# Performance work log

Measured on AMD Instinct MI355X. Metric: run time of the kernel, lower is better.

The kernel has to match this reference:

```python
import jax, jax.numpy as jnp
import numpy as np

D_MODEL = 384
D_STATE = 64
D_CONV = 3
EXPAND = 2
HEADDIM = 64
NGROUPS = 1
CHUNK = 256
D_INNER = EXPAND * D_MODEL            # 768
NHEADS = D_INNER // HEADDIM           # 12
CONV_DIM = D_INNER + 2 * NGROUPS * D_STATE   # 896
D_IN_PROJ = 2 * D_INNER + 2 * NGROUPS * D_STATE + NHEADS  # 1676
EPS = 1e-5


def setup_inputs() -> dict:
    key = jax.random.key(0)
    ks = jax.random.split(key, 8)
    B, H, W = 16, 32, 32
    u = jax.random.normal(ks[0], (B, D_MODEL, H, W), jnp.float32)
    in_proj_w = jax.random.normal(ks[1], (D_IN_PROJ, D_MODEL), jnp.float32) / np.sqrt(D_MODEL)
    conv_w = jax.random.normal(ks[2], (CONV_DIM, 1, D_CONV, D_CONV), jnp.float32) / np.sqrt(D_CONV * D_CONV)
    conv_b = jax.random.normal(ks[3], (CONV_DIM,), jnp.float32) * 0.01
    # dt_bias init as in Mamba2.__init__
    dt = jnp.exp(jax.random.uniform(ks[4], (NHEADS,)) * (np.log(0.1) - np.log(0.001)) + np.log(0.001))
    dt = jnp.clip(dt, 1e-4, None)
    dt_bias = dt + jnp.log(-jnp.expm1(-dt))
    A_log = jnp.log(jax.random.uniform(ks[5], (NHEADS,), minval=1.0, maxval=16.0))
    D = jnp.ones((NHEADS,), jnp.float32)
    norm_w = jnp.ones((D_INNER,), jnp.float32)
    norm_b = jnp.zeros((D_INNER,), jnp.float32)
    out_proj_w = jax.random.normal(ks[6], (D_MODEL, D_INNER), jnp.float32) / np.sqrt(D_INNER)
    return {"u": u, "in_proj_w": in_proj_w, "conv_w": conv_w, "conv_b": conv_b,
            "dt_bias": dt_bias, "A_log": A_log, "D": D, "norm_w": norm_w,
            "norm_b": norm_b, "out_proj_w": out_proj_w}


def _chunk_scan(x, dt, A, Bm, Cm):
    """SSD chunked scan. x:(b,l,h,p) dt:(b,l,h) A:(h,) Bm,Cm:(b,l,g,n) -> (b,l,h,p)"""
    b, l, h, p = x.shape
    nc = l // CHUNK
    xc = x.reshape(b, nc, CHUNK, h, p)
    dtc = dt.reshape(b, nc, CHUNK, h)
    hpg = h // NGROUPS
    Bh = jnp.repeat(Bm.reshape(b, nc, CHUNK, NGROUPS, D_STATE), hpg, axis=3)  # (b,c,cs,h,n)
    Ch = jnp.repeat(Cm.reshape(b, nc, CHUNK, NGROUPS, D_STATE), hpg, axis=3)
    dA = dtc * A                                  # (b,c,cs,h)
    dA_cs = jnp.cumsum(dA, axis=2)                # cumulative log-decay within chunk
    # ---- intra-chunk (masked, attention-like) ----
    Lmat = jnp.exp(dA_cs[:, :, :, None, :] - dA_cs[:, :, None, :, :])  # (b,c,i,j,h)
    causal = jnp.tril(jnp.ones((CHUNK, CHUNK), bool))
    att = jnp.einsum('bcihn,bcjhn->bcijh', Ch, Bh) * Lmat * dtc[:, :, None, :, :]
    att = jnp.where(causal[None, None, :, :, None], att, 0.0)
    y_intra = jnp.einsum('bcijh,bcjhp->bcihp', att, xc)
    # ---- per-chunk end states ----
    decay_to_end = jnp.exp(dA_cs[:, :, -1:, :] - dA_cs)                 # (b,c,cs,h)
    states = jnp.einsum('bcjhn,bcjh,bcjhp->bchpn', Bh, decay_to_end * dtc, xc)
    chunk_decay = jnp.exp(dA_cs[:, :, -1, :])                           # (b,c,h)
    # ---- inter-chunk recurrence over the (few) chunks ----
    def step(carry, inp):
        st, dec = inp
        new = carry * dec[:, :, None, None] + st
        return new, carry  # emit state *before* this chunk
    init = jnp.zeros((b, h, p, D_STATE), x.dtype)
    _, prevs = jax.lax.scan(step, init, (jnp.moveaxis(states, 1, 0), jnp.moveaxis(chunk_decay, 1, 0)))
    prev_states = jnp.moveaxis(prevs, 0, 1)                             # (b,c,h,p,n)
    y_inter = jnp.einsum('bcihn,bcih,bchpn->bcihp', Ch, jnp.exp(dA_cs), prev_states)
    return (y_intra + y_inter).reshape(b, l, h, p)


def reference(u, in_proj_w, conv_w, conv_b, dt_bias, A_log, D, norm_w, norm_b, out_proj_w):
    B, C, H, W = u.shape
    L = H * W
    useq = u.reshape(B, C, L).transpose(0, 2, 1)                        # (B,L,C)
    zxbcdt = useq @ in_proj_w.T                                         # (B,L,D_IN_PROJ)
    z = zxbcdt[..., :D_INNER]
    xBC = zxbcdt[..., D_INNER:D_INNER + CONV_DIM]
    dt = jax.nn.softplus(zxbcdt[..., D_INNER + CONV_DIM:] + dt_bias)    # (B,L,NHEADS)
    # depthwise 3x3 conv over (H,W)
    xBC = xBC.reshape(B, H, W, CONV_DIM)
    kern = jnp.transpose(conv_w, (2, 3, 1, 0))                          # HWIO, groups=CONV_DIM
    xBC = jax.lax.conv_general_dilated(xBC, kern, (1, 1), 'SAME',
                                       dimension_numbers=('NHWC', 'HWIO', 'NHWC'),
                                       feature_group_count=CONV_DIM) + conv_b
    xBC = jax.nn.silu(xBC).reshape(B, L, CONV_DIM)
    x = xBC[..., :D_INNER].reshape(B, L, NHEADS, HEADDIM)
    Bm = xBC[..., D_INNER:D_INNER + NGROUPS * D_STATE].reshape(B, L, NGROUPS, D_STATE)
    Cm = xBC[..., D_INNER + NGROUPS * D_STATE:].reshape(B, L, NGROUPS, D_STATE)
    A = -jnp.exp(A_log)
    y = _chunk_scan(x, dt, A, Bm, Cm) + D[None, None, :, None] * x      # D skip per head
    y = y.reshape(B, L, D_INNER)
    # LayerNorm then gate by z (no activation on z, matching source)
    mu = jnp.mean(y, axis=-1, keepdims=True)
    var = jnp.var(y, axis=-1, keepdims=True)
    y = (y - mu) / jnp.sqrt(var + EPS) * norm_w + norm_b
    y = y * z
    out = y @ out_proj_w.T                                              # (B,L,C)
    return out.reshape(B, H, W, C).transpose(0, 3, 1, 2)
```

## Files before the change

kernel.cpp:

```cpp
#include <hip/hip_runtime.h>
#include <hip/hip_bf16.h>

#define B_    16
#define L_    1024
#define DM    384
#define DIP   1676
#define NIP   1664
#define DI    768
#define CONVD 896
#define NH    12
#define HD    64
#define DS    64
#define NCH   4
#define CH    256
#define EPS_  1e-5f

typedef unsigned short u16;
typedef unsigned int   u32;
typedef __attribute__((ext_vector_type(8))) _Float16 f16x8;
typedef __attribute__((ext_vector_type(4))) float f32x4;

union U4 { uint4 v; u16 s[8]; };

#define SWZ(row, slot) (((row) << 7) + ((((slot) ^ ((row) & 7)) & 7) << 4))

__device__ __forceinline__ u16 f2h(float v) { return __builtin_bit_cast(u16, (_Float16)v); }
__device__ __forceinline__ float h2f(u16 h) { return (float)__builtin_bit_cast(_Float16, h); }
__device__ __forceinline__ void hsplit(float v, u16& h, u16& l) {
  _Float16 hh = (_Float16)v;
  _Float16 ll = (_Float16)(v - (float)hh);
  h = __builtin_bit_cast(u16, hh);
  l = __builtin_bit_cast(u16, ll);
}

__global__ __launch_bounds__(256) void k_cvtA(const float* __restrict__ u,
                                              u16* __restrict__ Ah)
{
  __shared__ float Ls[32][129];
  const int t  = threadIdx.x;
  const int l0 = blockIdx.x * 128;
  const int k0 = blockIdx.y * 32;
  const int b  = blockIdx.z;
#pragma unroll
  for (int r = 0; r < 4; ++r) {
    int idx = r * 256 + t;
    int kk = idx >> 5, q = idx & 31;
    float4 v = *(const float4*)&u[((size_t)(b * DM + k0 + kk)) * L_ + l0 + q * 4];
    Ls[kk][q * 4 + 0] = v.x; Ls[kk][q * 4 + 1] = v.y;
    Ls[kk][q * 4 + 2] = v.z; Ls[kk][q * 4 + 3] = v.w;
  }
  __syncthreads();
#pragma unroll
  for (int it = 0; it < 2; ++it) {
    int task = it * 256 + t;
    int l = task >> 2, kq = (task & 3) * 8;
    u32 hw[4];
#pragma unroll
    for (int j = 0; j < 4; ++j) {
      u16 h0 = f2h(Ls[kq + 2 * j + 0][l]);
      u16 h1 = f2h(Ls[kq + 2 * j + 1][l]);
      hw[j] = (u32)h0 | ((u32)h1 << 16);
    }
    size_t off = ((size_t)(b * L_ + l0 + l)) * DM + k0 + kq;
    *(uint4*)&Ah[off] = make_uint4(hw[0], hw[1], hw[2], hw[3]);
  }
}

__global__ __launch_bounds__(256) void k_cvtWh(const float* __restrict__ W,
                                               u16* __restrict__ Wh, int total4)
{
  int i = blockIdx.x * 256 + threadIdx.x;
  if (i >= total4) return;
  int e = i * 4;
  float4 v = *(const float4*)&W[e];
  u16 h[4] = {f2h(v.x), f2h(v.y), f2h(v.z), f2h(v.w)};
  *(uint2*)&Wh[e] = make_uint2((u32)h[0] | ((u32)h[1] << 16), (u32)h[2] | ((u32)h[3] << 16));
}

__global__ __launch_bounds__(256) void k_dtp(
    const float* __restrict__ u, const float* __restrict__ ipw,
    const float* __restrict__ dtb, const float* __restrict__ A_log,
    float* __restrict__ dt, float* __restrict__ dAcs, float* __restrict__ cdecay)
{
  __shared__ float wdt[DM];
  __shared__ float ws4[4];
  const int bc = blockIdx.x;
  const int h  = blockIdx.y;
  const int b  = bc >> 2, l0 = (bc & 3) * 256;
  const int t  = threadIdx.x;
  const int lane = t & 63, w = t >> 6;
  for (int i = t; i < DM; i += 256) wdt[i] = ipw[(size_t)(NIP + h) * DM + i];
  __syncthreads();
  const float* ub = u + (size_t)b * DM * L_ + l0 + t;
  float acc = 0.f;
#pragma unroll 8
  for (int k = 0; k < DM; ++k)
    acc = fmaf(ub[(size_t)k * L_], wdt[k], acc);
  const size_t row = (size_t)bc * 256 + t;
  float logit = acc + dtb[h];
  float dtv = (logit > 20.f) ? logit : log1pf(expf(logit));
  dt[row * NH + h] = dtv;
  float xv = dtv * (-expf(A_log[h]));
#pragma unroll
  for (int off = 1; off < 64; off <<= 1) {
    float y = __shfl_up(xv, off, 64);
    if (lane >= off) xv += y;
  }
  if (lane == 63) ws4[w] = xv;
  __syncthreads();
  float add = 0.f;
#pragma unroll
  for (int i = 0; i < 4; ++i) if (i < w) add += ws4[i];
  xv += add;
  dAcs[row * NH + h] = xv;
  if (t == 255) cdecay[bc * NH + h] = expf(xv);
}

#define STAGE2(bufbase, k0) do {                                                                \
  _Pragma("unroll")                                                                             \
  for (int i_ = 0; i_ < 2; ++i_) {                                                              \
    int S_ = i_ * 256 + t;                                                                      \
    int m_ = S_ >> 2;                                                                           \
    int g_ = (S_ ^ (m_ >> 1)) & 3;                                                              \
    size_t goff_ = (size_t)m_ * DM + (k0) + g_ * 8;                                             \
    __builtin_amdgcn_global_load_lds((const __attribute__((address_space(1))) u32*)(g0 + goff_),\
        (__attribute__((address_space(3))) u32*)(lds + (bufbase) + S_ * 8), 16, 0, 0);          \
    __builtin_amdgcn_global_load_lds((const __attribute__((address_space(1))) u32*)(g2 + goff_),\
        (__attribute__((address_space(3))) u32*)(lds + (bufbase) + 4096 + S_ * 8), 16, 0, 0);   \
  }                                                                                             \
} while (0)

__global__ __launch_bounds__(256) void k_gemm1(
    const u16* __restrict__ Ah,
    const u16* __restrict__ Wh,
    u16* __restrict__ z, u16* __restrict__ xBC)
{
  __shared__ u16 lds[16384];
  const int t = threadIdx.x;
  const int lane = t & 63, wid = t >> 6;
  const int wr = wid >> 1, wc = wid & 1;
  const int gg = lane >> 4, mlo = lane & 15;
  const int xs = (blockIdx.x & 7) * 16 + (blockIdx.x >> 3);
  const int m0 = xs * 128, n0 = blockIdx.y * 128;
  f32x4 acc[4][4];
#pragma unroll
  for (int i = 0; i < 4; ++i)
#pragma unroll
    for (int j = 0; j < 4; ++j) acc[i][j] = (f32x4){0.f, 0.f, 0.f, 0.f};
  const u16* g0 = Ah + (size_t)m0 * DM;
  const u16* g2 = Wh + (size_t)n0 * DM;
  const int NT = DM / 32;
  STAGE2(0, 0);
  int cur = 0;
  for (int kt = 0; kt < NT; ++kt) {
    int ks = kt + 1; if (ks > NT - 1) ks = NT - 1;
    STAGE2((cur ^ 1) * 8192, ks * 32);
    asm volatile("s_waitcnt vmcnt(4)" ::: "memory");
    __builtin_amdgcn_s_barrier();
    const char* ldsb = (const char*)lds + cur * 16384;
    f16x8 fa[4], fb[4];
#pragma unroll
    for (int mf = 0; mf < 4; ++mf) {
      int m = wr * 64 + mf * 16 + mlo;
      int off = m * 64 + (((gg ^ (m >> 1)) & 3) << 4);
      fa[mf]  = *(const f16x8*)(ldsb + off);
    }
#pragma unroll
    for (int nf = 0; nf < 4; ++nf) {
      int n = wc * 64 + nf * 16 + mlo;
      int off = n * 64 + (((gg ^ (n >> 1)) & 3) << 4);
      fb[nf]  = *(const f16x8*)(ldsb + 8192 + off);
    }
#pragma unroll
    for (int mf = 0; mf < 4; ++mf)
#pragma unroll
      for (int nf = 0; nf < 4; ++nf)
        acc[mf][nf] = __builtin_amdgcn_mfma_f32_16x16x32_f16(fa[mf], fb[nf], acc[mf][nf], 0, 0, 0);
    __builtin_amdgcn_s_barrier();
    cur ^= 1;
  }
  const int rb = m0 + wr * 64 + (lane >> 4) * 4;
  const int cb = n0 + wc * 64 + mlo;
#pragma unroll
  for (int mf = 0; mf < 4; ++mf)
#pragma unroll
    for (int nf = 0; nf < 4; ++nf) {
      int col = cb + nf * 16;
#pragma unroll
      for (int r = 0; r < 4; ++r) {
        int row = rb + mf * 16 + r;
        float v = acc[mf][nf][r];
        if (col < DI) z[(size_t)row * DI + col] = f2h(v);
        else xBC[(size_t)row * CONVD + (col - DI)] = f2h(v);
      }
    }
}

#define STAGE3B(bufbase, k0) do {                                                               \
  _Pragma("unroll")                                                                             \
  for (int i_ = 0; i_ < 2; ++i_) {                                                              \
    int S_ = i_ * 256 + t;                                                                      \
    int m_ = S_ >> 2;                                                                           \
    int g_ = (S_ ^ (m_ >> 1)) & 3;                                                              \
    size_t goff_ = (size_t)m_ * DI + (k0) + g_ * 8;                                             \
    __builtin_amdgcn_global_load_lds((const __attribute__((address_space(1))) u32*)(g0 + goff_),\
        (__attribute__((address_space(3))) u32*)(lds + (bufbase) + S_ * 8), 16, 0, 0);          \
    __builtin_amdgcn_global_load_lds((const __attribute__((address_space(1))) u32*)(g1 + goff_),\
        (__attribute__((address_space(3))) u32*)(lds + (bufbase) + 4096 + S_ * 8), 16, 0, 0);   \
    __builtin_amdgcn_global_load_lds((const __attribute__((address_space(1))) u32*)(g2 + goff_),\
        (__attribute__((address_space(3))) u32*)(lds + (bufbase) + 8192 + S_ * 8), 16, 0, 0);   \
  }                                                                                             \
} while (0)

__global__ __launch_bounds__(256) void k_gemm2(
    const u16* __restrict__ Ah, const u16* __restrict__ Al,
    const u16* __restrict__ Bh,
    float* __restrict__ out)
{
  __shared__ u16 lds[24576];
  const int t = threadIdx.x;
  const int lane = t & 63, wid = t >> 6;
  const int wr = wid >> 1, wc = wid & 1;
  const int gg = lane >> 4, mlo = lane & 15;
  const int xs = (blockIdx.x & 7) * 16 + (blockIdx.x >> 3);
  const int m0 = xs * 128, n0 = blockIdx.y * 128;
  f32x4 acc[4][4];
#pragma unroll
  for (int i = 0; i < 4; ++i)
#pragma unroll
    for (int j = 0; j < 4; ++j) acc[i][j] = (f32x4){0.f, 0.f, 0.f, 0.f};
  const u16* g0 = Ah + (size_t)m0 * DI;
  const u16* g1 = Al + (size_t)m0 * DI;
  const u16* g2 = Bh + (size_t)n0 * DI;
  const int NT = DI / 32;
  STAGE3B(0, 0);
  int cur = 0;
  for (int kt = 0; kt < NT; ++kt) {
    int ks = kt + 1; if (ks > NT - 1) ks = NT - 1;
    STAGE3B((cur ^ 1) * 12288, ks * 32);
    asm volatile("s_waitcnt vmcnt(6)" ::: "memory");
    __builtin_amdgcn_s_barrier();
    const char* ldsb = (const char*)lds + cur * 24576;
    f16x8 fa[4], fal[4], fb[4];
#pragma unroll
    for (int mf = 0; mf < 4; ++mf) {
      int m = wr * 64 + mf * 16 + mlo;
      int off = m * 64 + (((gg ^ (m >> 1)) & 3) << 4);
      fa[mf]  = *(const f16x8*)(ldsb + off);
      fal[mf] = *(const f16x8*)(ldsb + 8192 + off);
    }
#pragma unroll
    for (int nf = 0; nf < 4; ++nf) {
      int n = wc * 64 + nf * 16 + mlo;
      int off = n * 64 + (((gg ^ (n >> 1)) & 3) << 4);
      fb[nf]  = *(const f16x8*)(ldsb + 16384 + off);
    }
#pragma unroll
    for (int mf = 0; mf < 4; ++mf)
#pragma unroll
      for (int nf = 0; nf < 4; ++nf) {
        acc[mf][nf] = __builtin_amdgcn_mfma_f32_16x16x32_f16(fa[mf],  fb[nf], acc[mf][nf], 0, 0, 0);
        acc[mf][nf] = __builtin_amdgcn_mfma_f32_16x16x32_f16(fal[mf], fb[nf], acc[mf][nf], 0, 0, 0);
      }
    __builtin_amdgcn_s_barrier();
    cur ^= 1;
  }
  const int rb = m0 + wr * 64 + (lane >> 4) * 4;
  const int cb = n0 + wc * 64 + mlo;
#pragma unroll
  for (int mf = 0; mf < 4; ++mf)
#pragma unroll
    for (int nf = 0; nf < 4; ++nf) {
      int col = cb + nf * 16;
#pragma unroll
      for (int r = 0; r < 4; ++r) {
        int row = rb + mf * 16 + r;
        int b = row >> 10, l = row & 1023;
        out[((size_t)(b * DM + col)) * L_ + l] = acc[mf][nf][r];
      }
    }
}

#define CC 16
__global__ __launch_bounds__(256) void k_conv(
    const u16* __restrict__ xBC, const float* __restrict__ cw,
    const float* __restrict__ cb,
    u16* __restrict__ XTh,
    u16* __restrict__ Bh,
    u16* __restrict__ Chh)
{
  __shared__ float Ls[18][32][CC];
  const int t  = threadIdx.x;
  const int c0 = blockIdx.x * CC;
  const int h0 = blockIdx.y * 16;
  const int b  = blockIdx.z;
#pragma unroll
  for (int k = 0; k < 9; ++k) {
    int f = k * 256 + t;
    int fc4 = f & 3, fw = (f >> 2) & 31, fr = f >> 7;
    int h = h0 + fr - 1;
    U4 v; v.v = make_uint4(0, 0, 0, 0);
    if (h >= 0 && h < 32) {
      uint2 p = *(const uint2*)&xBC[((size_t)(b * 1024 + h * 32 + fw)) * CONVD + c0 + fc4 * 4];
      v.v.x = p.x; v.v.y = p.y;
    }
    Ls[fr][fw][fc4 * 4 + 0] = h2f(v.s[0]);
    Ls[fr][fw][fc4 * 4 + 1] = h2f(v.s[1]);
    Ls[fr][fw][fc4 * 4 + 2] = h2f(v.s[2]);
    Ls[fr][fw][fc4 * 4 + 3] = h2f(v.s[3]);
  }
  const int c4 = t & 3;
  const int w  = (t >> 2) & 31;
  const int hb = t >> 7;
  float wt[4][9];
  float bias[4];
#pragma unroll
  for (int j = 0; j < 4; ++j) {
    int c = c0 + c4 * 4 + j;
    bias[j] = cb[c];
#pragma unroll
    for (int kb = 0; kb < 9; ++kb) wt[j][kb] = cw[c * 9 + kb];
  }
  __syncthreads();
  const bool isx = (c0 < DI);
  u16 xh16[8][4];
#pragma unroll
  for (int k = 0; k < 8; ++k) {
    int h = hb * 8 + k;
    float acc[4] = {bias[0], bias[1], bias[2], bias[3]};
#pragma unroll
    for (int dh = 0; dh < 3; ++dh) {
#pragma unroll
      for (int dw = -1; dw <= 1; ++dw) {
        int ww = w + dw;
        if (ww < 0 || ww > 31) continue;
        const float* p = &Ls[h + dh][ww][c4 * 4];
        int kb = dh * 3 + (dw + 1);
#pragma unroll
        for (int j = 0; j < 4; ++j) acc[j] = fmaf(p[j], wt[j][kb], acc[j]);
      }
    }
    float s4[4];
#pragma unroll
    for (int j = 0; j < 4; ++j) { float v = acc[j]; s4[j] = v / (1.f + expf(-v)); }
    if (isx) {
#pragma unroll
      for (int j = 0; j < 4; ++j) xh16[k][j] = f2h(s4[j]);
    } else {
      size_t row = (size_t)b * 1024 + (h0 + h) * 32 + w;
      u16 hv[4] = {f2h(s4[0]), f2h(s4[1]), f2h(s4[2]), f2h(s4[3])};
      uint2 hp = make_uint2((u32)hv[0] | ((u32)hv[1] << 16), (u32)hv[2] | ((u32)hv[3] << 16));
      int c = c0 + c4 * 4;
      if (c < DI + DS) *(uint2*)&Bh[row * DS + (c - DI)] = hp;
      else             *(uint2*)&Chh[row * DS + (c - DI - DS)] = hp;
    }
  }
  if (isx) {
    __syncthreads();
    u16* Ls2 = (u16*)Ls;
#pragma unroll
    for (int k = 0; k < 8; ++k) {
      int pos = (hb * 8 + k) * 32 + w;
#pragma unroll
      for (int j = 0; j < 4; ++j)
        Ls2[(c4 * 4 + j) * 512 + pos] = xh16[k][j];
    }
    __syncthreads();
    const int hh = c0 >> 6;
    const int pb = c0 & 63;
#pragma unroll
    for (int i = 0; i < 4; ++i) {
      int cid = i * 256 + t;
      int pl = cid >> 6, rem = cid & 63;
      int jbl = rem >> 3, slot = rem & 7;
      int labs = h0 * 32 + jbl * 64;
      size_t tile = ((size_t)(b * 4 + (labs >> 8)) * NH + hh) * 4 + ((labs >> 6) & 3);
      *(uint4*)((char*)XTh + tile * 8192 + SWZ(pb + pl, slot)) =
          *(const uint4*)&Ls2[pl * 512 + jbl * 64 + slot * 8];
    }
  }
}

#define STAGE_XT(tileByte) do {                                                                   \
  _Pragma("unroll")                                                                               \
  for (int i_ = 0; i_ < 2; ++i_) {                                                                \
    int S_ = i_ * 256 + t;                                                                        \
    __builtin_amdgcn_global_load_lds(                                                             \
        (const __attribute__((address_space(1))) u32*)((const char*)XTh + (tileByte) + S_ * 16),  \
        (__attribute__((address_space(3))) u32*)((char*)Xh_t + S_ * 16), 16, 0, 0);               \
  }                                                                                               \
} while (0)

__global__ __launch_bounds__(256) void k_states(
    const u16* __restrict__ XTh,
    const u16* __restrict__ Bh,
    const float* __restrict__ dt, const float* __restrict__ dAcs,
    float* __restrict__ states)
{
  __shared__ u16 bpackB[64 * 65];
  __shared__ u16 BTh_t[4096];
  __shared__ u16 Xh_t[4096];
  __shared__ float wall[256];
  const int bc = blockIdx.x;
  const int hh = blockIdx.y;
  const int t  = threadIdx.x;
  const int lane = t & 63, w = t >> 6;
  const int mlo = lane & 15, gg = lane >> 4;
  const int r = t >> 2, q = (t & 3) * 16;
  const size_t base = (size_t)bc * 256;
  const float last = dAcs[(base + 255) * NH + hh];
  wall[t] = __expf(last - dAcs[(base + t) * NH + hh]) * dt[(base + t) * NH + hh];
  f32x4 acc[4];
#pragma unroll
  for (int i = 0; i < 4; ++i) acc[i] = (f32x4){0.f, 0.f, 0.f, 0.f};
  for (int jt = 0; jt < 4; ++jt) {
    const int j0 = jt * 64;
    __syncthreads();
    STAGE_XT(((size_t)(bc * NH + hh) * 4 + jt) * 8192);
    {
      const u16* bhp = &Bh[(size_t)(base + j0 + r) * DS + q];
      U4 H0, H1;
      H0.v = *(const uint4*)bhp; H1.v = *(const uint4*)(bhp + 8);
#pragma unroll
      for (int k = 0; k < 8; ++k) {
        bpackB[r * 65 + q + k]     = H0.s[k];
        bpackB[r * 65 + q + 8 + k] = H1.s[k];
      }
    }
    __syncthreads();
#pragma unroll
    for (int c = 0; c < 2; ++c) {
      U4 BH;
#pragma unroll
      for (int jj = 0; jj < 8; ++jj) {
        int j = q + c * 8 + jj;
        BH.s[jj] = f2h(h2f(bpackB[j * 65 + r]) * wall[j0 + j]);
      }
      *(uint4*)((char*)BTh_t + SWZ(r, (q >> 3) + c)) = BH.v;
    }
    __syncthreads();
#pragma unroll
    for (int s = 0; s < 2; ++s) {
      f16x8 fah = *(const f16x8*)((const char*)Xh_t + SWZ(w * 16 + mlo, s * 4 + gg));
#pragma unroll
      for (int nf = 0; nf < 4; ++nf) {
        f16x8 fbh = *(const f16x8*)((const char*)BTh_t + SWZ(nf * 16 + mlo, s * 4 + gg));
        acc[nf] = __builtin_amdgcn_mfma_f32_16x16x32_f16(fah, fbh, acc[nf], 0, 0, 0);
      }
    }
  }
  const size_t sb = ((size_t)(bc * NH + hh)) << 12;
#pragma unroll
  for (int nf = 0; nf < 4; ++nf)
#pragma unroll
    for (int reg = 0; reg < 4; ++reg) {
      int p = w * 16 + (lane >> 4) * 4 + reg;
      int n = nf * 16 + mlo;
      states[sb + (size_t)p * 64 + n] = acc[nf][reg];
    }
}

__global__ __launch_bounds__(256) void k_scanc(
    const float* __restrict__ states, const float* __restrict__ cdecay,
    float* __restrict__ prev)
{
  int tid = blockIdx.x * 256 + threadIdx.x;
  int pn  = tid & 4095;
  int rem = tid >> 12;
  int hh  = rem % NH;
  int b   = rem / NH;
  float carry = 0.f;
#pragma unroll
  for (int c = 0; c < 4; ++c) {
    size_t idx = ((size_t)((b * 4 + c) * NH + hh) << 12) + pn;
    prev[idx] = carry;
    carry = carry * cdecay[(b * 4 + c) * NH + hh] + states[idx];
  }
}

__global__ __launch_bounds__(256) void k_y(
    const u16* __restrict__ XTh,
    const u16* __restrict__ Chg, const u16* __restrict__ Bhg,
    const float* __restrict__ dtp, const float* __restrict__ dAcs,
    const float* __restrict__ prev, const float* __restrict__ Dp,
    u16* __restrict__ y)
{
  __shared__ u16 Pb_t[4096];
  __shared__ u16 Xh_t[4096];
  __shared__ u16 att_t[4096];
  __shared__ float dAc_s[256], dt_s[256], ei_s[128];
  const int bc = blockIdx.x;
  const int hh = blockIdx.y;
  const int z  = blockIdx.z;
  const int it0 = z * 2;
  const int t  = threadIdx.x;
  const int lane = t & 63, w = t >> 6;
  const int mlo = lane & 15, gg = lane >> 4;
  const int r = t >> 2, q = (t & 3) * 16;
  const int slot0 = q >> 3;
  const size_t base = (size_t)bc * 256;
  {
    float da = dAcs[(base + t) * NH + hh];
    dAc_s[t] = da;
    dt_s[t]  = dtp[(base + t) * NH + hh];
    if (t < 128) ei_s[t] = __expf(dAcs[(base + z * 128 + t) * NH + hh]);
  }
  {
    const float* pp = &prev[(((size_t)(bc * NH + hh)) << 12) + (size_t)r * 64 + q];
    U4 H0, H1;
#pragma unroll
    for (int k = 0; k < 16; ++k) {
      u16 h = f2h(pp[k]);
      if (k < 8) H0.s[k] = h; else H1.s[k - 8] = h;
    }
    *(uint4*)((char*)Pb_t + SWZ(r, slot0))     = H0.v;
    *(uint4*)((char*)Pb_t + SWZ(r, slot0 + 1)) = H1.v;
  }
  __syncthreads();
  f16x8 fc[2][2];
#pragma unroll
  for (int iti = 0; iti < 2; ++iti)
#pragma unroll
    for (int s = 0; s < 2; ++s)
      fc[iti][s] = *(const f16x8*)&Chg[(size_t)(base + (it0 + iti) * 64 + w * 16 + mlo) * DS +
                                       (s * 4 + gg) * 8];
  f32x4 accy[2][4];
#pragma unroll
  for (int i = 0; i < 2; ++i)
#pragma unroll
    for (int j = 0; j < 4; ++j) accy[i][j] = (f32x4){0.f, 0.f, 0.f, 0.f};
#pragma unroll
  for (int s = 0; s < 2; ++s)
#pragma unroll
    for (int pf = 0; pf < 4; ++pf) {
      f16x8 fph = *(const f16x8*)((const char*)Pb_t + SWZ(pf * 16 + mlo, s * 4 + gg));
#pragma unroll
      for (int iti = 0; iti < 2; ++iti)
        accy[iti][pf] = __builtin_amdgcn_mfma_f32_16x16x32_f16(fc[iti][s], fph, accy[iti][pf], 0, 0, 0);
    }
  const int ilb = w * 16 + (lane >> 4) * 4;
#pragma unroll
  for (int iti = 0; iti < 2; ++iti)
#pragma unroll
    for (int pf = 0; pf < 4; ++pf)
#pragma unroll
      for (int reg = 0; reg < 4; ++reg)
        accy[iti][pf][reg] *= ei_s[iti * 64 + ilb + reg];

  u32 xdv[2][8];
  for (int jt = 0; jt <= it0 + 1; ++jt) {
    __syncthreads();
    STAGE_XT(((size_t)(bc * NH + hh) * 4 + jt) * 8192);
    {
      const u16* bh = &Bhg[(size_t)(base + jt * 64 + r) * DS + q];
      U4 V0, V1;
      V0.v = *(const uint4*)bh; V1.v = *(const uint4*)(bh + 8);
      float wj = dt_s[jt * 64 + r];
#pragma unroll
      for (int k = 0; k < 8; ++k) {
        V0.s[k] = f2h(h2f(V0.s[k]) * wj);
        V1.s[k] = f2h(h2f(V1.s[k]) * wj);
      }
      *(uint4*)((char*)Pb_t + SWZ(r, slot0))     = V0.v;
      *(uint4*)((char*)Pb_t + SWZ(r, slot0 + 1)) = V1.v;
    }
    __syncthreads();
#pragma unroll
    for (int iti = 0; iti < 2; ++iti) {
      if (jt == it0 + iti) {
#pragma unroll
        for (int pf = 0; pf < 4; ++pf)
#pragma unroll
          for (int rp = 0; rp < 2; ++rp) {
            int j0l = ilb + rp * 2;
            u16 a = *(const u16*)((const char*)Xh_t + SWZ(pf * 16 + mlo, j0l >> 3) + (j0l & 7) * 2);
            u16 b2 = *(const u16*)((const char*)Xh_t + SWZ(pf * 16 + mlo, (j0l + 1) >> 3) + ((j0l + 1) & 7) * 2);
            xdv[iti][pf * 2 + rp] = (u32)a | ((u32)b2 << 16);
          }
      }
    }
#pragma unroll
    for (int iti = 0; iti < 2; ++iti) {
      const int ita = it0 + iti;
      if (jt > ita) continue;
      f32x4 g[4];
#pragma unroll
      for (int i = 0; i < 4; ++i) g[i] = (f32x4){0.f, 0.f, 0.f, 0.f};
#pragma unroll
      for (int s = 0; s < 2; ++s)
#pragma unroll
        for (int jf = 0; jf < 4; ++jf) {
          f16x8 fbh = *(const f16x8*)((const char*)Pb_t + SWZ(jf * 16 + mlo, s * 4 + gg));
          g[jf] = __builtin_amdgcn_mfma_f32_16x16x32_f16(fc[iti][s], fbh, g[jf], 0, 0, 0);
        }
#pragma unroll
      for (int jf = 0; jf < 4; ++jf)
#pragma unroll
        for (int reg = 0; reg < 4; ++reg) {
          int il = ita * 64 + ilb + reg;
          int jl = jt * 64 + jf * 16 + mlo;
          float av = (jl <= il) ? g[jf][reg] * __expf(dAc_s[il] - dAc_s[jl]) : 0.f;
          *(u16*)((char*)att_t + SWZ(il & 63, (jl & 63) >> 3) + (jl & 7) * 2) = f2h(av);
        }
#pragma unroll
      for (int s = 0; s < 2; ++s) {
        f16x8 fa = *(const f16x8*)((const char*)att_t + SWZ(w * 16 + mlo, s * 4 + gg));
#pragma unroll
        for (int pf = 0; pf < 4; ++pf) {
          f16x8 fxh = *(const f16x8*)((const char*)Xh_t + SWZ(pf * 16 + mlo, s * 4 + gg));
          accy[iti][pf] = __builtin_amdgcn_mfma_f32_16x16x32_f16(fa, fxh, accy[iti][pf], 0, 0, 0);
        }
      }
    }
  }
  const float Dh = Dp[hh];
#pragma unroll
  for (int iti = 0; iti < 2; ++iti)
#pragma unroll
    for (int pf = 0; pf < 4; ++pf)
#pragma unroll
      for (int reg = 0; reg < 4; ++reg) {
        size_t row = base + (it0 + iti) * 64 + ilb + reg;
        int col = hh * HD + pf * 16 + mlo;
        u32 pk = xdv[iti][pf * 2 + (reg >> 1)];
        u16 xv = (reg & 1) ? (u16)(pk >> 16) : (u16)pk;
        y[row * DI + col] = f2h(accy[iti][pf][reg] + Dh * h2f(xv));
      }
}

__global__ __launch_bounds__(256) void k_norm(
    const u16* __restrict__ z, const float* __restrict__ nw,
    const float* __restrict__ nb, const u16* __restrict__ y,
    u16* __restrict__ yh, u16* __restrict__ yl)
{
  __shared__ float rs[4], rq[4];
  const size_t row = blockIdx.x;
  const int t = threadIdx.x;
  float v[3];
  float s = 0.f, sq = 0.f;
#pragma unroll
  for (int r = 0; r < 3; ++r) {
    v[r] = h2f(y[row * DI + r * 256 + t]);
    s += v[r];
    sq = fmaf(v[r], v[r], sq);
  }
#pragma unroll
  for (int off = 32; off > 0; off >>= 1) {
    s  += __shfl_down(s, off, 64);
    sq += __shfl_down(sq, off, 64);
  }
  const int wid = t >> 6, lane = t & 63;
  if (lane == 0) { rs[wid] = s; rq[wid] = sq; }
  __syncthreads();
  if (t == 0) {
    rs[0] = rs[0] + rs[1] + rs[2] + rs[3];
    rq[0] = rq[0] + rq[1] + rq[2] + rq[3];
  }
  __syncthreads();
  const float mu   = rs[0] * (1.f / DI);
  const float var  = rq[0] * (1.f / DI) - mu * mu;
  const float rstd = 1.f / sqrtf(var + EPS_);
#pragma unroll
  for (int r = 0; r < 3; ++r) {
    int d = r * 256 + t;
    float o = (v[r] - mu) * rstd * nw[d] + nb[d];
    float p = o * h2f(z[row * DI + d]);
    u16 h, l;
    hsplit(p, h, l);
    yh[row * DI + d] = h;
    yl[row * DI + d] = l;
  }
}

extern "C" void kernel_launch(void* const* d_in, const int* in_sizes, int n_in,
                              void* d_out, int out_size, void* d_ws, size_t ws_size,
                              hipStream_t stream)
{
  const float* u    = (const float*)d_in[0];
  const float* ipw  = (const float*)d_in[1];
  const float* cw   = (const float*)d_in[2];
  const float* cb   = (const float*)d_in[3];
  const float* dtb  = (const float*)d_in[4];
  const float* Alog = (const float*)d_in[5];
  const float* Dp   = (const float*)d_in[6];
  const float* nw   = (const float*)d_in[7];
  const float* nb   = (const float*)d_in[8];
  const float* opw  = (const float*)d_in[9];
  float* out = (float*)d_out;

  float* ws = (float*)d_ws;
  size_t off = 0;
  u16*   z16     = (u16*)(ws + off); off += (size_t)B_ * L_ * DI / 2;
  u16*   xBC16   = (u16*)(ws + off); off += (size_t)B_ * L_ * CONVD / 2;
  float* dt_buf  = ws + off; off += (size_t)B_ * L_ * NH;
  float* x_buf   = ws + off; off += (size_t)B_ * L_ * DI;
  u16*   y16     = (u16*)(ws + off); off += (size_t)B_ * L_ * DI / 2;
  u16*   Bh_buf  = (u16*)(ws + off); off += (size_t)B_ * L_ * DS / 2;
  u16*   Ch_buf  = (u16*)(ws + off); off += (size_t)B_ * L_ * DS / 2;
  float* dAcs    = ws + off; off += (size_t)B_ * L_ * NH;
  float* cdec    = ws + off; off += (size_t)B_ * NCH * NH;
  float* st_buf  = ws + off; off += (size_t)B_ * NCH * NH * HD * DS;
  float* pv_buf  = ws + off; off += (size_t)B_ * NCH * NH * HD * DS;
  u16*   Woh     = (u16*)(ws + off); off += (size_t)DM * DI / 2;
  u16*   XTh_buf = (u16*)(ws + off); off += (size_t)B_ * NCH * NH * 4 * 4096 / 2;

  u16* Ah = (u16*)x_buf;
  u16* Whip = Ah + (size_t)B_ * L_ * DM;
  u16* yh = (u16*)x_buf;
  u16* yl = yh + (size_t)B_ * L_ * DI;

  hipLaunchKernelGGL(k_cvtA, dim3(8, 12, 16), dim3(256), 0, stream, u, Ah);
  hipLaunchKernelGGL(k_cvtWh, dim3((NIP * DM / 4 + 255) / 256), dim3(256), 0, stream,
                     ipw, Whip, NIP * DM / 4);
  hipLaunchKernelGGL(k_cvtWh, dim3((DM * DI / 4 + 255) / 256), dim3(256), 0, stream,
                     opw, Woh, DM * DI / 4);
  hipLaunchKernelGGL(k_dtp, dim3(64, 12), dim3(256), 0, stream,
                     u, ipw, dtb, Alog, dt_buf, dAcs, cdec);
  hipLaunchKernelGGL(k_gemm1, dim3(128, 13), dim3(256), 0, stream,
                     Ah, Whip, z16, xBC16);
  hipLaunchKernelGGL(k_conv, dim3(56, 2, 16), dim3(256), 0, stream,
                     xBC16, cw, cb, XTh_buf, Bh_buf, Ch_buf);
  hipLaunchKernelGGL(k_states, dim3(64, 12), dim3(256), 0, stream,
                     XTh_buf, Bh_buf, dt_buf, dAcs, st_buf);
  hipLaunchKernelGGL(k_scanc, dim3(3072), dim3(256), 0, stream, st_buf, cdec, pv_buf);
  hipLaunchKernelGGL(k_y, dim3(64, 12, 2), dim3(256), 0, stream,
                     XTh_buf, Ch_buf, Bh_buf, dt_buf, dAcs, pv_buf, Dp, y16);
  hipLaunchKernelGGL(k_norm, dim3(16384), dim3(256), 0, stream, z16, nw, nb, y16, yh, yl);
  hipLaunchKernelGGL(k_gemm2, dim3(128, 3), dim3(256), 0, stream, yh, yl, Woh, out);
}
```

Baseline: 203.6 us.

## Merge prep kernels into one launch and enlarge gemm1 tile to 256x128

Four small preprocessing kernels (activation fp16 transpose, two weight casts, dt projection/cumsum) are merged into one launch that picks a role from the block index, cutting launch gaps. The in_proj GEMM moves from 128x128 tiles to 256x128 tiles, with each wave owning 64 rows across all 128 columns. This raises operand reuse per LDS load and halves the grid. In exchange it doubles accumulator registers, which may lower occupancy, and 832 blocks may fill the CUs less evenly.

```diff
diff --git a/kernel.cpp b/kernel.cpp
--- a/kernel.cpp
+++ b/kernel.cpp
@@ -33,100 +33,114 @@
   l = __builtin_bit_cast(u16, ll);
 }
 
-__global__ __launch_bounds__(256) void k_cvtA(const float* __restrict__ u,
-                                              u16* __restrict__ Ah)
-{
-  __shared__ float Ls[32][129];
-  const int t  = threadIdx.x;
-  const int l0 = blockIdx.x * 128;
-  const int k0 = blockIdx.y * 32;
-  const int b  = blockIdx.z;
-#pragma unroll
-  for (int r = 0; r < 4; ++r) {
-    int idx = r * 256 + t;
-    int kk = idx >> 5, q = idx & 31;
-    float4 v = *(const float4*)&u[((size_t)(b * DM + k0 + kk)) * L_ + l0 + q * 4];
-    Ls[kk][q * 4 + 0] = v.x; Ls[kk][q * 4 + 1] = v.y;
-    Ls[kk][q * 4 + 2] = v.z; Ls[kk][q * 4 + 3] = v.w;
-  }
-  __syncthreads();
-#pragma unroll
-  for (int it = 0; it < 2; ++it) {
-    int task = it * 256 + t;
-    int l = task >> 2, kq = (task & 3) * 8;
-    u32 hw[4];
-#pragma unroll
-    for (int j = 0; j < 4; ++j) {
-      u16 h0 = f2h(Ls[kq + 2 * j + 0][l]);
-      u16 h1 = f2h(Ls[kq + 2 * j + 1][l]);
-      hw[j] = (u32)h0 | ((u32)h1 << 16);
-    }
-    size_t off = ((size_t)(b * L_ + l0 + l)) * DM + k0 + kq;
-    *(uint4*)&Ah[off] = make_uint4(hw[0], hw[1], hw[2], hw[3]);
-  }
-}
-
-__global__ __launch_bounds__(256) void k_cvtWh(const float* __restrict__ W,
-                                               u16* __restrict__ Wh, int total4)
-{
-  int i = blockIdx.x * 256 + threadIdx.x;
-  if (i >= total4) return;
-  int e = i * 4;
-  float4 v = *(const float4*)&W[e];
-  u16 h[4] = {f2h(v.x), f2h(v.y), f2h(v.z), f2h(v.w)};
-  *(uint2*)&Wh[e] = make_uint2((u32)h[0] | ((u32)h[1] << 16), (u32)h[2] | ((u32)h[3] << 16));
-}
-
-__global__ __launch_bounds__(256) void k_dtp(
+__global__ __launch_bounds__(256) void k_prep(
     const float* __restrict__ u, const float* __restrict__ ipw,
+    const float* __restrict__ opw,
     const float* __restrict__ dtb, const float* __restrict__ A_log,
+    u16* __restrict__ Ah, u16* __restrict__ Whip, u16* __restrict__ Woh,
     float* __restrict__ dt, float* __restrict__ dAcs, float* __restrict__ cdecay)
 {
-  __shared__ float wdt[DM];
-  __shared__ float ws4[4];
-  const int bc = blockIdx.x;
-  const int h  = blockIdx.y;
-  const int b  = bc >> 2, l0 = (bc & 3) * 256;
-  const int t  = threadIdx.x;
-  const int lane = t & 63, w = t >> 6;
-  for (int i = t; i < DM; i += 256) wdt[i] = ipw[(size_t)(NIP + h) * DM + i];
-  __syncthreads();
-  const float* ub = u + (size_t)b * DM * L_ + l0 + t;
-  float acc = 0.f;
+  __shared__ float smem[32 * 129 + 8];
+  const int bid = blockIdx.x;
+  const int t = threadIdx.x;
+  if (bid < 1536) {
+    float (*Ls)[129] = (float(*)[129])smem;
+    const int l0 = (bid & 7) * 128;
+    const int k0 = ((bid >> 3) % 12) * 32;
+    const int b  = bid / 96;
+#pragma unroll
+    for (int r = 0; r < 4; ++r) {
+      int idx = r * 256 + t;
+      int kk = idx >> 5, q = idx & 31;
+      float4 v = *(const float4*)&u[((size_t)(b * DM + k0 + kk)) * L_ + l0 + q * 4];
+      Ls[kk][q * 4 + 0] = v.x; Ls[kk][q * 4 + 1] = v.y;
+      Ls[kk][q * 4 + 2] = v.z; Ls[kk][q * 4 + 3] = v.w;
+    }
+    __syncthreads();
+#pragma unroll
+    for (int it = 0; it < 2; ++it) {
+      int task = it * 256 + t;
+      int l = task >> 2, kq = (task & 3) * 8;
+      u32 hw[4];
+#pragma unroll
+      for (int j = 0; j < 4; ++j) {
+        u16 h0 = f2h(Ls[kq + 2 * j + 0][l]);
+        u16 h1 = f2h(Ls[kq + 2 * j + 1][l]);
+        hw[j] = (u32)h0 | ((u32)h1 << 16);
+      }
+      size_t off = ((size_t)(b * L_ + l0 + l)) * DM + k0 + kq;
+      *(uint4*)&Ah[off] = make_uint4(hw[0], hw[1], hw[2], hw[3]);
+    }
+  } else if (bid < 2160) {
+    int i = (bid - 1536) * 256 + t;
+    if (i < NIP * DM / 4) {
+      int e = i * 4;
+      float4 v = *(const float4*)&ipw[e];
+      u16 h[4] = {f2h(v.x), f2h(v.y), f2h(v.z), f2h(v.w)};
+      *(uint2*)&Whip[e] = make_uint2((u32)h[0] | ((u32)h[1] << 16), (u32)h[2] | ((u32)h[3] << 16));
+    }
+  } else if (bid < 2448) {
+    int i = (bid - 2160) * 256 + t;
+    if (i < DM * DI / 4) {
+      int e = i * 4;
+      float4 v = *(const float4*)&opw[e];
+      u16 h[4] = {f2h(v.x), f2h(v.y), f2h(v.z), f2h(v.w)};
+      *(uint2*)&Woh[e] = make_uint2((u32)h[0] | ((u32)h[1] << 16), (u32)h[2] | ((u32)h[3] << 16));
+    }
+  } else {
+    float* wdt = smem;
+    float* ws4 = smem + DM;
+    const int bb = bid - 2448;
+    const int bc = bb & 63;
+    const int h  = bb >> 6;
+    const int b  = bc >> 2, l0 = (bc & 3) * 256;
+    const int lane = t & 63, w = t >> 6;
+    for (int i = t; i < DM; i += 256) wdt[i] = ipw[(size_t)(NIP + h) * DM + i];
+    __syncthreads();
+    const float* ub = u + (size_t)b * DM * L_ + l0 + t;
+    float acc = 0.f;
 #pragma unroll 8
-  for (int k = 0; k < DM; ++k)
-    acc = fmaf(ub[(size_t)k * L_], wdt[k], acc);
-  const size_t row = (size_t)bc * 256 + t;
-  float logit = acc + dtb[h];
-  float dtv = (logit > 20.f) ? logit : log1pf(expf(logit));
-  dt[row * NH + h] = dtv;
-  float xv = dtv * (-expf(A_log[h]));
-#pragma unroll
-  for (int off = 1; off < 64; off <<= 1) {
-    float y = __shfl_up(xv, off, 64);
-    if (lane >= off) xv += y;
-  }
-  if (lane == 63) ws4[w] = xv;
-  __syncthreads();
-  float add = 0.f;
-#pragma unroll
-  for (int i = 0; i < 4; ++i) if (i < w) add += ws4[i];
-  xv += add;
-  dAcs[row * NH + h] = xv;
-  if (t == 255) cdecay[bc * NH + h] = expf(xv);
-}
-
-#define STAGE2(bufbase, k0) do {                                                                \
+    for (int k = 0; k < DM; ++k)
+      acc = fmaf(ub[(size_t)k * L_], wdt[k], acc);
+    const size_t row = (size_t)bc * 256 + t;
+    float logit = acc + dtb[h];
+    float dtv = (logit > 20.f) ? logit : log1pf(expf(logit));
+    dt[row * NH + h] = dtv;
+    float xv = dtv * (-expf(A_log[h]));
+#pragma unroll
+    for (int off = 1; off < 64; off <<= 1) {
+      float y = __shfl_up(xv, off, 64);
+      if (lane >= off) xv += y;
+    }
+    if (lane == 63) ws4[w] = xv;
+    __syncthreads();
+    float add = 0.f;
+#pragma unroll
+    for (int i = 0; i < 4; ++i) if (i < w) add += ws4[i];
+    xv += add;
+    dAcs[row * NH + h] = xv;
+    if (t == 255) cdecay[bc * NH + h] = expf(xv);
+  }
+}
+
+#define STAGE_AB(bufbase, k0) do {                                                              \
   _Pragma("unroll")                                                                             \
-  for (int i_ = 0; i_ < 2; ++i_) {                                                              \
+  for (int i_ = 0; i_ < 4; ++i_) {                                                              \
     int S_ = i_ * 256 + t;                                                                      \
     int m_ = S_ >> 2;                                                                           \
     int g_ = (S_ ^ (m_ >> 1)) & 3;                                                              \
     size_t goff_ = (size_t)m_ * DM + (k0) + g_ * 8;                                             \
     __builtin_amdgcn_global_load_lds((const __attribute__((address_space(1))) u32*)(g0 + goff_),\
         (__attribute__((address_space(3))) u32*)(lds + (bufbase) + S_ * 8), 16, 0, 0);          \
+  }                                                                                             \
+  _Pragma("unroll")                                                                             \
+  for (int i_ = 0; i_ < 2; ++i_) {                                                              \
+    int S_ = i_ * 256 + t;                                                                      \
+    int n_ = S_ >> 2;                                                                           \
+    int g_ = (S_ ^ (n_ >> 1)) & 3;                                                              \
+    size_t goff_ = (size_t)n_ * DM + (k0) + g_ * 8;                                             \
     __builtin_amdgcn_global_load_lds((const __attribute__((address_space(1))) u32*)(g2 + goff_),\
-        (__attribute__((address_space(3))) u32*)(lds + (bufbase) + 4096 + S_ * 8), 16, 0, 0);   \
+        (__attribute__((address_space(3))) u32*)(lds + (bufbase) + 8192 + S_ * 8), 16, 0, 0);   \
   }                                                                                             \
 } while (0)
 
@@ -135,57 +149,55 @@
     const u16* __restrict__ Wh,
     u16* __restrict__ z, u16* __restrict__ xBC)
 {
-  __shared__ u16 lds[16384];
+  __shared__ u16 lds[24576];
   const int t = threadIdx.x;
   const int lane = t & 63, wid = t >> 6;
-  const int wr = wid >> 1, wc = wid & 1;
   const int gg = lane >> 4, mlo = lane & 15;
-  const int xs = (blockIdx.x & 7) * 16 + (blockIdx.x >> 3);
-  const int m0 = xs * 128, n0 = blockIdx.y * 128;
-  f32x4 acc[4][4];
+  const int xs = (blockIdx.x & 7) * 8 + (blockIdx.x >> 3);
+  const int m0 = xs * 256, n0 = blockIdx.y * 128;
+  f32x4 acc[4][8];
 #pragma unroll
   for (int i = 0; i < 4; ++i)
 #pragma unroll
-    for (int j = 0; j < 4; ++j) acc[i][j] = (f32x4){0.f, 0.f, 0.f, 0.f};
+    for (int j = 0; j < 8; ++j) acc[i][j] = (f32x4){0.f, 0.f, 0.f, 0.f};
   const u16* g0 = Ah + (size_t)m0 * DM;
   const u16* g2 = Wh + (size_t)n0 * DM;
   const int NT = DM / 32;
-  STAGE2(0, 0);
+  STAGE_AB(0, 0);
   int cur = 0;
   for (int kt = 0; kt < NT; ++kt) {
     int ks = kt + 1; if (ks > NT - 1) ks = NT - 1;
-    STAGE2((cur ^ 1) * 8192, ks * 32);
-    asm volatile("s_waitcnt vmcnt(4)" ::: "memory");
+    STAGE_AB((cur ^ 1) * 12288, ks * 32);
+    asm volatile("s_waitcnt vmcnt(6)" ::: "memory");
     __builtin_amdgcn_s_barrier();
-    const char* ldsb = (const char*)lds + cur * 16384;
-    f16x8 fa[4], fb[4];
+    const char* ldsb = (const char*)lds + cur * 24576;
+    f16x8 fa[4], fb[8];
 #pragma unroll
     for (int mf = 0; mf < 4; ++mf) {
-      int m = wr * 64 + mf * 16 + mlo;
+      int m = wid * 64 + mf * 16 + mlo;
       int off = m * 64 + (((gg ^ (m >> 1)) & 3) << 4);
-      fa[mf]  = *(const f16x8*)(ldsb + off);
-    }
-#pragma unroll
-    for (int nf = 0; nf < 4; ++nf) {
-      int n = wc * 64 + nf * 16 + mlo;
+      fa[mf] = *(const f16x8*)(ldsb + off);
+    }
+#pragma unroll
+    for (int nf = 0; nf < 8; ++nf) {
+      int n = nf * 16 + mlo;
       int off = n * 64 + (((gg ^ (n >> 1)) & 3) << 4);
-      fb[nf]  = *(const f16x8*)(ldsb + 8192 + off);
+      fb[nf] = *(const f16x8*)(ldsb + 16384 + off);
     }
 #pragma unroll
     for (int mf = 0; mf < 4; ++mf)
 #pragma unroll
-      for (int nf = 0; nf < 4; ++nf)
+      for (int nf = 0; nf < 8; ++nf)
         acc[mf][nf] = __builtin_amdgcn_mfma_f32_16x16x32_f16(fa[mf], fb[nf], acc[mf][nf], 0, 0, 0);
     __builtin_amdgcn_s_barrier();
     cur ^= 1;
   }
-  const int rb = m0 + wr * 64 + (lane >> 4) * 4;
-  const int cb = n0 + wc * 64 + mlo;
+  const int rb = m0 + wid * 64 + (lane >> 4) * 4;
 #pragma unroll
   for (int mf = 0; mf < 4; ++mf)
 #pragma unroll
-    for (int nf = 0; nf < 4; ++nf) {
-      int col = cb + nf * 16;
+    for (int nf = 0; nf < 8; ++nf) {
+      int col = n0 + nf * 16 + mlo;
 #pragma unroll
       for (int r = 0; r < 4; ++r) {
         int row = rb + mf * 16 + r;
@@ -709,14 +721,9 @@
   u16* yh = (u16*)x_buf;
   u16* yl = yh + (size_t)B_ * L_ * DI;
 
-  hipLaunchKernelGGL(k_cvtA, dim3(8, 12, 16), dim3(256), 0, stream, u, Ah);
-  hipLaunchKernelGGL(k_cvtWh, dim3((NIP * DM / 4 + 255) / 256), dim3(256), 0, stream,
-                     ipw, Whip, NIP * DM / 4);
-  hipLaunchKernelGGL(k_cvtWh, dim3((DM * DI / 4 + 255) / 256), dim3(256), 0, stream,
-                     opw, Woh, DM * DI / 4);
-  hipLaunchKernelGGL(k_dtp, dim3(64, 12), dim3(256), 0, stream,
-                     u, ipw, dtb, Alog, dt_buf, dAcs, cdec);
-  hipLaunchKernelGGL(k_gemm1, dim3(128, 13), dim3(256), 0, stream,
+  hipLaunchKernelGGL(k_prep, dim3(3216), dim3(256), 0, stream,
+                     u, ipw, opw, dtb, Alog, Ah, Whip, Woh, dt_buf, dAcs, cdec);
+  hipLaunchKernelGGL(k_gemm1, dim3(64, 13), dim3(256), 0, stream,
                      Ah, Whip, z16, xBC16);
   hipLaunchKernelGGL(k_conv, dim3(56, 2, 16), dim3(256), 0, stream,
                      xBC16, cw, cb, XTh_buf, Bh_buf, Ch_buf);
```

Result: slower. 214.0 us (+5.1%).
